# Optimization experiments

Hardware: AMD Instinct MI355X
Metric: run time of the kernel (lower is better)

The kernel has to match this reference:

```python
import jax, jax.numpy as jnp
import numpy as np

N_USERS = 200000
N_ITEMS = 100000
EMB_DIM = 64
N_LAYERS = 3
N_EDGES = 4000000
N_TOTAL = N_USERS + N_ITEMS


def setup_inputs() -> dict:
    key = jax.random.key(0)
    k1, k2, k3, k4 = jax.random.split(key, 4)
    # Xavier-uniform-ish init scale for embeddings
    lim = float(np.sqrt(6.0 / (N_USERS + EMB_DIM)))
    user_w = jax.random.uniform(k1, (N_USERS, EMB_DIM), jnp.float32, -lim, lim)
    lim_i = float(np.sqrt(6.0 / (N_ITEMS + EMB_DIM)))
    item_w = jax.random.uniform(k2, (N_ITEMS, EMB_DIM), jnp.float32, -lim_i, lim_i)
    src = jax.random.randint(k3, (N_EDGES,), 0, N_TOTAL, dtype=jnp.int32)
    dst = jax.random.randint(k4, (N_EDGES,), 0, N_TOTAL, dtype=jnp.int32)
    return {"user_w": user_w, "item_w": item_w, "src": src, "dst": dst}


def reference(user_w, item_w, src, dst):
    # x: [N_TOTAL, D] joint node embedding table
    x = jnp.concatenate([user_w, item_w], axis=0)
    # Row-degree of the COO adjacency (duplicates sum, same as coalesce)
    deg = jax.ops.segment_sum(jnp.ones_like(src, dtype=x.dtype), src,
                              num_segments=N_TOTAL)
    deg_inv_sqrt = jax.lax.rsqrt(deg + 1e-8)
    # Symmetric normalization weight per edge: d_i^-1/2 * d_j^-1/2
    w = (deg_inv_sqrt[src] * deg_inv_sqrt[dst])[:, None]  # [E, 1]

    h = x
    acc = x
    for _ in range(N_LAYERS):
        # SpMM: out[i] = sum_{(i,j) in E} w_ij * h[j]
        h = jax.ops.segment_sum(w * h[dst], src, num_segments=N_TOTAL)
        acc = acc + h
    out = acc / (N_LAYERS + 1)
    return out[:N_USERS], out[N_USERS:]
```

## Files before the change

kernel.cpp:

```cpp
#include <hip/hip_runtime.h>

#define N_USERS  200000
#define N_ITEMS  100000
#define N_TOTAL  300000
#define EMB_DIM  64
#define N_EDGES  4000000
#define N_LAYERS 3

#define SCAN_CHUNK 1024

#define B2_BITS 9
#define B2_ROWS (1 << B2_BITS)
#define NB2 ((N_TOTAL + B2_ROWS - 1) >> B2_BITS)
#define CHUNK_E 8192
#define NBLK ((N_EDGES + CHUNK_E - 1) / CHUNK_E)
#define NFLAT (NB2 * NBLK)
#define NSB_FLAT ((NFLAT + SCAN_CHUNK - 1) / SCAN_CHUNK)

#define DST_BITS 19
#define DST_MASK ((1 << DST_BITS) - 1)

typedef float f32x2 __attribute__((ext_vector_type(2)));

__device__ __forceinline__ unsigned bfpack(float a, float b) {
    unsigned ua = __float_as_uint(a); ua = (ua + 0x7fffu + ((ua >> 16) & 1u)) >> 16;
    unsigned ub = __float_as_uint(b); ub = (ub + 0x7fffu + ((ub >> 16) & 1u)) >> 16;
    return ua | (ub << 16);
}
__device__ __forceinline__ float bflo(unsigned u) { return __uint_as_float(u << 16); }
__device__ __forceinline__ float bfhi(unsigned u) { return __uint_as_float(u & 0xffff0000u); }
__device__ __forceinline__ f32x2 bf2(unsigned u) {
    f32x2 t; t.x = bflo(u); t.y = bfhi(u); return t;
}

__global__ void scanA_g(const int* __restrict__ in, int* __restrict__ out,
                        int* __restrict__ bsums, int n) {
    __shared__ int lds[256];
    int t = threadIdx.x, b = blockIdx.x;
    int base = b * SCAN_CHUNK + t * 4;
    int v[4];
#pragma unroll
    for (int k = 0; k < 4; ++k)
        v[k] = (base + k < n) ? in[base + k] : 0;
    int s = v[0] + v[1] + v[2] + v[3];
    lds[t] = s;
    __syncthreads();
    for (int off = 1; off < 256; off <<= 1) {
        int x = (t >= off) ? lds[t - off] : 0;
        __syncthreads();
        lds[t] += x;
        __syncthreads();
    }
    int inc = lds[t];
    int exc = inc - s;
    if (t == 255) bsums[b] = inc;
    int run = exc;
#pragma unroll
    for (int k = 0; k < 4; ++k) {
        if (base + k < n) out[base + k] = run;
        run += v[k];
    }
}

__global__ void scanB_g(int* __restrict__ bsums, int nb, int* __restrict__ total_out) {
    __shared__ int lds[512];
    int t = threadIdx.x;
    int v = (t < nb) ? bsums[t] : 0;
    lds[t] = v;
    __syncthreads();
    for (int o = 1; o < 512; o <<= 1) {
        int x = (t >= o) ? lds[t - o] : 0;
        __syncthreads();
        lds[t] += x;
        __syncthreads();
    }
    if (t < nb) bsums[t] = lds[t] - v;
    if (total_out && t == nb - 1) *total_out = lds[t];
}

__global__ __launch_bounds__(512) void partA_kernel(const int* __restrict__ src,
                                                    int* __restrict__ bcnt) {
    __shared__ int lcnt[NB2];
    int blk = blockIdx.x, t = threadIdx.x;
    for (int i = t; i < NB2; i += 512) lcnt[i] = 0;
    __syncthreads();
    int base = blk * CHUNK_E;
    int end = base + CHUNK_E; if (end > N_EDGES) end = N_EDGES;
    for (int e = base + 4 * t; e < end; e += 4 * 512) {
        int4 s4 = *(const int4*)(src + e);
        atomicAdd(&lcnt[s4.x >> B2_BITS], 1);
        atomicAdd(&lcnt[s4.y >> B2_BITS], 1);
        atomicAdd(&lcnt[s4.z >> B2_BITS], 1);
        atomicAdd(&lcnt[s4.w >> B2_BITS], 1);
    }
    __syncthreads();
    for (int i = t; i < NB2; i += 512)
        bcnt[(size_t)i * NBLK + blk] = lcnt[i];
}

__global__ __launch_bounds__(512) void partC_kernel(const int* __restrict__ src,
                                                    const int* __restrict__ dst,
                                                    const int* __restrict__ boffs,
                                                    const int* __restrict__ bs2,
                                                    int* __restrict__ edgebuf) {
    __shared__ int lcur[NB2];
    int blk = blockIdx.x, t = threadIdx.x;
    for (int i = t; i < NB2; i += 512) {
        size_t f = (size_t)i * NBLK + blk;
        lcur[i] = boffs[f] + bs2[f >> 10];
    }
    __syncthreads();
    int base = blk * CHUNK_E;
    int end = base + CHUNK_E; if (end > N_EDGES) end = N_EDGES;
    for (int e = base + 2 * t; e < end; e += 2 * 512) {
        int2 s2 = *(const int2*)(src + e);
        int2 d2 = *(const int2*)(dst + e);
        int pos0 = atomicAdd(&lcur[s2.x >> B2_BITS], 1);
        edgebuf[pos0] = ((s2.x & (B2_ROWS - 1)) << DST_BITS) | d2.x;
        int pos1 = atomicAdd(&lcur[s2.y >> B2_BITS], 1);
        edgebuf[pos1] = ((s2.y & (B2_ROWS - 1)) << DST_BITS) | d2.y;
    }
}

__global__ __launch_bounds__(512) void part2_kernel(const int* __restrict__ boffs,
                                                    const int* __restrict__ bs2,
                                                    const int* __restrict__ edgebuf,
                                                    int* __restrict__ col,
                                                    int* __restrict__ offs,
                                                    float* __restrict__ dinv) {
    __shared__ int lhist[B2_ROWS];
    __shared__ int lsums[512];
    int b = blockIdx.x;
    int base = b << B2_BITS;
    int nrows = N_TOTAL - base; if (nrows > B2_ROWS) nrows = B2_ROWS;
    int t = threadIdx.x;
    size_t f0 = (size_t)b * NBLK;
    int bstart = boffs[f0] + bs2[f0 >> 10];
    int eend;
    if (b + 1 < NB2) {
        size_t f1 = (size_t)(b + 1) * NBLK;
        eend = boffs[f1] + bs2[f1 >> 10];
    } else eend = N_EDGES;

    if (t < B2_ROWS) lhist[t] = 0;
    __syncthreads();
    for (int j = bstart + t; j < eend; j += 512)
        atomicAdd(&lhist[edgebuf[j] >> DST_BITS], 1);
    __syncthreads();
    int v = lhist[t];
    lsums[t] = v;
    __syncthreads();
    for (int o = 1; o < 512; o <<= 1) {
        int x = (t >= o) ? lsums[t - o] : 0;
        __syncthreads();
        lsums[t] += x;
        __syncthreads();
    }
    int o0 = bstart + lsums[t] - v;
    if (t < nrows) {
        offs[base + t] = o0;
        dinv[base + t] = rsqrtf((float)v + 1e-8f);
    }
    if (b == NB2 - 1 && t == 0) offs[N_TOTAL] = N_EDGES;
    lhist[t] = o0;
    __syncthreads();
    for (int j = bstart + t; j < eend; j += 512) {
        int e = edgebuf[j];
        int pos = atomicAdd(&lhist[e >> DST_BITS], 1);
        col[pos] = e & DST_MASK;
    }
}

__global__ void convert_kernel(const float4* __restrict__ uw4,
                               const float4* __restrict__ iw4,
                               const float* __restrict__ dinv,
                               uint2* __restrict__ g0) {
    int i = blockIdx.x * blockDim.x + threadIdx.x;
    const int n = (N_TOTAL + 1) * 16;
    if (i < n) {
        int row = i >> 4;
        if (row >= N_TOTAL) {
            g0[i] = make_uint2(0u, 0u);
        } else {
            float4 x = (row < N_USERS) ? uw4[i] : iw4[i - N_USERS * 16];
            float di = dinv[row];
            g0[i] = make_uint2(bfpack(di * x.x, di * x.y),
                               bfpack(di * x.z, di * x.w));
        }
    }
}

template <int MODE>
__global__ __launch_bounds__(256) void gather_kernel(
        const int* __restrict__ offs,
        const int* __restrict__ col,
        const float* __restrict__ dinv,
        const unsigned* __restrict__ gprev,
        unsigned* __restrict__ gnext,
        float4* __restrict__ out4,
        const float4* __restrict__ uw4,
        const float4* __restrict__ iw4) {
    int row  = blockIdx.x * 4 + (threadIdx.x >> 6);
    int lane = threadIdx.x & 63;
    int q    = lane >> 4;
    int r    = lane & 15;
    int start = __builtin_amdgcn_readfirstlane(offs[row]);
    int end   = __builtin_amdgcn_readfirstlane(offs[row + 1]);
    float di  = dinv[row];
    f32x2 acc01 = {0.f, 0.f};
    f32x2 acc23 = {0.f, 0.f};
    for (int cb = start; cb < end; cb += 64) {
        int rem = end - cb;
        int n = rem > 64 ? 64 : rem;
        int myc = (lane < rem) ? col[cb + lane] : N_TOTAL;
        for (int k0 = 0; k0 < n; k0 += 16) {
            int c0 = __shfl(myc, k0 + q);
            int c1 = __shfl(myc, k0 + 4 + q);
            int c2 = __shfl(myc, k0 + 8 + q);
            int c3 = __shfl(myc, k0 + 12 + q);
            uint2 u0 = *(const uint2*)(gprev + ((size_t)(unsigned)c0 << 5) + 2 * r);
            uint2 u1 = *(const uint2*)(gprev + ((size_t)(unsigned)c1 << 5) + 2 * r);
            uint2 u2 = *(const uint2*)(gprev + ((size_t)(unsigned)c2 << 5) + 2 * r);
            uint2 u3 = *(const uint2*)(gprev + ((size_t)(unsigned)c3 << 5) + 2 * r);
            acc01 += bf2(u0.x); acc23 += bf2(u0.y);
            acc01 += bf2(u1.x); acc23 += bf2(u1.y);
            acc01 += bf2(u2.x); acc23 += bf2(u2.y);
            acc01 += bf2(u3.x); acc23 += bf2(u3.y);
        }
    }
    float a0 = acc01.x, a1 = acc01.y, a2 = acc23.x, a3 = acc23.y;
    a0 += __shfl_xor(a0, 16);
    a1 += __shfl_xor(a1, 16);
    a2 += __shfl_xor(a2, 16);
    a3 += __shfl_xor(a3, 16);
    a0 += __shfl_xor(a0, 32);
    a1 += __shfl_xor(a1, 32);
    a2 += __shfl_xor(a2, 32);
    a3 += __shfl_xor(a3, 32);
    if (lane < 16) {
        float h0 = di * a0, h1 = di * a1, h2 = di * a2, h3 = di * a3;
        int p = row * 16 + r;
        if (MODE == 0) {
            float4 x = (row < N_USERS) ? uw4[p] : iw4[p - N_USERS * 16];
            ((uint2*)gnext)[p] = make_uint2(bfpack(di * h0, di * h1),
                                            bfpack(di * h2, di * h3));
            out4[p] = make_float4(x.x + h0, x.y + h1, x.z + h2, x.w + h3);
        } else if (MODE == 1) {
            float4 o = out4[p];
            ((uint2*)gnext)[p] = make_uint2(bfpack(di * h0, di * h1),
                                            bfpack(di * h2, di * h3));
            out4[p] = make_float4(o.x + h0, o.y + h1, o.z + h2, o.w + h3);
        } else {
            float4 o = out4[p];
            out4[p] = make_float4((o.x + h0) * 0.25f, (o.y + h1) * 0.25f,
                                  (o.z + h2) * 0.25f, (o.w + h3) * 0.25f);
        }
    }
    if (MODE != 2) {
        if (blockIdx.x == 0 && threadIdx.x < 32)
            gnext[N_TOTAL * 32 + threadIdx.x] = 0u;
    }
}

extern "C" void kernel_launch(void* const* d_in, const int* in_sizes, int n_in,
                              void* d_out, int out_size, void* d_ws, size_t ws_size,
                              hipStream_t stream) {
    const float* user_w = (const float*)d_in[0];
    const float* item_w = (const float*)d_in[1];
    const int*   src    = (const int*)d_in[2];
    const int*   dst    = (const int*)d_in[3];
    float* out = (float*)d_out;
    (void)in_sizes; (void)n_in; (void)out_size; (void)ws_size;

    char* ws = (char*)d_ws;
    size_t off = 0;
    auto alloc = [&](size_t bytes) {
        char* p = ws + off;
        off = (off + bytes + 255) & ~(size_t)255;
        return p;
    };
    int*      offs   = (int*)     alloc((size_t)(N_TOTAL + 1) * 4);
    int*      bcnt   = (int*)     alloc((size_t)NFLAT * 4);
    int*      boffs  = (int*)     alloc((size_t)NFLAT * 4);
    int*      bs2    = (int*)     alloc((size_t)NSB_FLAT * 4);
    int*      col    = (int*)     alloc((size_t)N_EDGES * 4);
    int*      edgebuf= (int*)     alloc((size_t)N_EDGES * 4);
    float*    dinv   = (float*)   alloc((size_t)N_TOTAL * 4);
    unsigned* g0     = (unsigned*)alloc((size_t)(N_TOTAL + 1) * 32 * 4);
    unsigned* g_a    = (unsigned*)alloc((size_t)(N_TOTAL + 1) * 32 * 4);
    unsigned* g_b    = (unsigned*)alloc((size_t)(N_TOTAL + 1) * 32 * 4);

    const int B = 256;
    const int gatherGrid = N_TOTAL / 4;

    partA_kernel<<<NBLK, 512, 0, stream>>>(src, bcnt);
    scanA_g<<<NSB_FLAT, B, 0, stream>>>(bcnt, boffs, bs2, NFLAT);
    scanB_g<<<1, 512, 0, stream>>>(bs2, NSB_FLAT, nullptr);
    partC_kernel<<<NBLK, 512, 0, stream>>>(src, dst, boffs, bs2, edgebuf);
    part2_kernel<<<NB2, 512, 0, stream>>>(boffs, bs2, edgebuf, col, offs, dinv);

    convert_kernel<<<((N_TOTAL + 1) * 16 + B - 1) / B, B, 0, stream>>>(
        (const float4*)user_w, (const float4*)item_w, dinv, (uint2*)g0);

    const float4* uw4 = (const float4*)user_w;
    const float4* iw4 = (const float4*)item_w;
    float4* out4 = (float4*)out;
    gather_kernel<0><<<gatherGrid, B, 0, stream>>>(offs, col, dinv, g0,  g_a, out4, uw4, iw4);
    gather_kernel<1><<<gatherGrid, B, 0, stream>>>(offs, col, dinv, g_a, g_b, out4, uw4, iw4);
    gather_kernel<2><<<gatherGrid, B, 0, stream>>>(offs, col, dinv, g_b, nullptr, out4, uw4, iw4);
}
```

Baseline: 573.9 us.

## Process four rows per wavefront with prefetched column indices; stage bucket edges in LDS

The gather kernel now assigns four consecutive rows to each wavefront, loading all row offsets and degree factors at once and prefetching the next row's column indices while the current row is processed. This is meant to hide the latency of the col load and offset reads that came before each row's feature gathers. Separately, part2 caches a bucket's edges in shared memory when they fit, so the second pass reads LDS instead of re-reading edgebuf from global memory. The costs are fewer waves in flight (grid reduced fourfold), more registers, and a 40KB LDS allocation in part2 that may lower its occupancy.

```diff
diff --git a/kernel.cpp b/kernel.cpp
--- a/kernel.cpp
+++ b/kernel.cpp
@@ -19,6 +19,10 @@
 
 #define DST_BITS 19
 #define DST_MASK ((1 << DST_BITS) - 1)
+
+#define P2_CAP 10240
+
+#define GR 4
 
 typedef float f32x2 __attribute__((ext_vector_type(2)));
 
@@ -130,6 +134,7 @@
                                                     float* __restrict__ dinv) {
     __shared__ int lhist[B2_ROWS];
     __shared__ int lsums[512];
+    __shared__ int lbuf[P2_CAP];
     int b = blockIdx.x;
     int base = b << B2_BITS;
     int nrows = N_TOTAL - base; if (nrows > B2_ROWS) nrows = B2_ROWS;
@@ -141,11 +146,21 @@
         size_t f1 = (size_t)(b + 1) * NBLK;
         eend = boffs[f1] + bs2[f1 >> 10];
     } else eend = N_EDGES;
+    int cnt = eend - bstart;
+    bool fits = (cnt <= P2_CAP);
 
     if (t < B2_ROWS) lhist[t] = 0;
     __syncthreads();
-    for (int j = bstart + t; j < eend; j += 512)
-        atomicAdd(&lhist[edgebuf[j] >> DST_BITS], 1);
+    if (fits) {
+        for (int j = t; j < cnt; j += 512) {
+            int e = edgebuf[bstart + j];
+            lbuf[j] = e;
+            atomicAdd(&lhist[e >> DST_BITS], 1);
+        }
+    } else {
+        for (int j = bstart + t; j < eend; j += 512)
+            atomicAdd(&lhist[edgebuf[j] >> DST_BITS], 1);
+    }
     __syncthreads();
     int v = lhist[t];
     lsums[t] = v;
@@ -164,10 +179,18 @@
     if (b == NB2 - 1 && t == 0) offs[N_TOTAL] = N_EDGES;
     lhist[t] = o0;
     __syncthreads();
-    for (int j = bstart + t; j < eend; j += 512) {
-        int e = edgebuf[j];
-        int pos = atomicAdd(&lhist[e >> DST_BITS], 1);
-        col[pos] = e & DST_MASK;
+    if (fits) {
+        for (int j = t; j < cnt; j += 512) {
+            int e = lbuf[j];
+            int pos = atomicAdd(&lhist[e >> DST_BITS], 1);
+            col[pos] = e & DST_MASK;
+        }
+    } else {
+        for (int j = bstart + t; j < eend; j += 512) {
+            int e = edgebuf[j];
+            int pos = atomicAdd(&lhist[e >> DST_BITS], 1);
+            col[pos] = e & DST_MASK;
+        }
     }
 }
 
@@ -200,24 +223,37 @@
         float4* __restrict__ out4,
         const float4* __restrict__ uw4,
         const float4* __restrict__ iw4) {
-    int row  = blockIdx.x * 4 + (threadIdx.x >> 6);
+    int wid  = blockIdx.x * 4 + (threadIdx.x >> 6);
+    int base_row = wid * GR;
     int lane = threadIdx.x & 63;
     int q    = lane >> 4;
     int r    = lane & 15;
-    int start = __builtin_amdgcn_readfirstlane(offs[row]);
-    int end   = __builtin_amdgcn_readfirstlane(offs[row + 1]);
-    float di  = dinv[row];
-    f32x2 acc01 = {0.f, 0.f};
-    f32x2 acc23 = {0.f, 0.f};
-    for (int cb = start; cb < end; cb += 64) {
-        int rem = end - cb;
-        int n = rem > 64 ? 64 : rem;
-        int myc = (lane < rem) ? col[cb + lane] : N_TOTAL;
+    int li = lane < GR ? lane : GR;
+    int off_l = offs[base_row + li];
+    float dv  = dinv[base_row + (lane < GR ? lane : GR - 1)];
+
+    int s0 = __builtin_amdgcn_readlane(off_l, 0);
+    int e0 = __builtin_amdgcn_readlane(off_l, 1);
+    int myc_cur = (lane < e0 - s0) ? col[s0 + lane] : N_TOTAL;
+
+#pragma unroll
+    for (int i = 0; i < GR; ++i) {
+        int start = __builtin_amdgcn_readlane(off_l, i);
+        int end   = __builtin_amdgcn_readlane(off_l, i + 1);
+        int myc_next = N_TOTAL;
+        if (i + 1 < GR) {
+            int sn = __builtin_amdgcn_readlane(off_l, i + 1);
+            int en = __builtin_amdgcn_readlane(off_l, i + 2);
+            myc_next = (lane < en - sn) ? col[sn + lane] : N_TOTAL;
+        }
+        f32x2 acc01 = {0.f, 0.f};
+        f32x2 acc23 = {0.f, 0.f};
+        int n = end - start; if (n > 64) n = 64;
         for (int k0 = 0; k0 < n; k0 += 16) {
-            int c0 = __shfl(myc, k0 + q);
-            int c1 = __shfl(myc, k0 + 4 + q);
-            int c2 = __shfl(myc, k0 + 8 + q);
-            int c3 = __shfl(myc, k0 + 12 + q);
+            int c0 = __shfl(myc_cur, k0 + q);
+            int c1 = __shfl(myc_cur, k0 + 4 + q);
+            int c2 = __shfl(myc_cur, k0 + 8 + q);
+            int c3 = __shfl(myc_cur, k0 + 12 + q);
             uint2 u0 = *(const uint2*)(gprev + ((size_t)(unsigned)c0 << 5) + 2 * r);
             uint2 u1 = *(const uint2*)(gprev + ((size_t)(unsigned)c1 << 5) + 2 * r);
             uint2 u2 = *(const uint2*)(gprev + ((size_t)(unsigned)c2 << 5) + 2 * r);
@@ -227,34 +263,56 @@
             acc01 += bf2(u2.x); acc23 += bf2(u2.y);
             acc01 += bf2(u3.x); acc23 += bf2(u3.y);
         }
-    }
-    float a0 = acc01.x, a1 = acc01.y, a2 = acc23.x, a3 = acc23.y;
-    a0 += __shfl_xor(a0, 16);
-    a1 += __shfl_xor(a1, 16);
-    a2 += __shfl_xor(a2, 16);
-    a3 += __shfl_xor(a3, 16);
-    a0 += __shfl_xor(a0, 32);
-    a1 += __shfl_xor(a1, 32);
-    a2 += __shfl_xor(a2, 32);
-    a3 += __shfl_xor(a3, 32);
-    if (lane < 16) {
-        float h0 = di * a0, h1 = di * a1, h2 = di * a2, h3 = di * a3;
-        int p = row * 16 + r;
-        if (MODE == 0) {
-            float4 x = (row < N_USERS) ? uw4[p] : iw4[p - N_USERS * 16];
-            ((uint2*)gnext)[p] = make_uint2(bfpack(di * h0, di * h1),
-                                            bfpack(di * h2, di * h3));
-            out4[p] = make_float4(x.x + h0, x.y + h1, x.z + h2, x.w + h3);
-        } else if (MODE == 1) {
-            float4 o = out4[p];
-            ((uint2*)gnext)[p] = make_uint2(bfpack(di * h0, di * h1),
-                                            bfpack(di * h2, di * h3));
-            out4[p] = make_float4(o.x + h0, o.y + h1, o.z + h2, o.w + h3);
-        } else {
-            float4 o = out4[p];
-            out4[p] = make_float4((o.x + h0) * 0.25f, (o.y + h1) * 0.25f,
-                                  (o.z + h2) * 0.25f, (o.w + h3) * 0.25f);
-        }
+        for (int cb = start + 64; cb < end; cb += 64) {
+            int rem = end - cb;
+            int nn = rem > 64 ? 64 : rem;
+            int myc = (lane < rem) ? col[cb + lane] : N_TOTAL;
+            for (int k0 = 0; k0 < nn; k0 += 16) {
+                int c0 = __shfl(myc, k0 + q);
+                int c1 = __shfl(myc, k0 + 4 + q);
+                int c2 = __shfl(myc, k0 + 8 + q);
+                int c3 = __shfl(myc, k0 + 12 + q);
+                uint2 u0 = *(const uint2*)(gprev + ((size_t)(unsigned)c0 << 5) + 2 * r);
+                uint2 u1 = *(const uint2*)(gprev + ((size_t)(unsigned)c1 << 5) + 2 * r);
+                uint2 u2 = *(const uint2*)(gprev + ((size_t)(unsigned)c2 << 5) + 2 * r);
+                uint2 u3 = *(const uint2*)(gprev + ((size_t)(unsigned)c3 << 5) + 2 * r);
+                acc01 += bf2(u0.x); acc23 += bf2(u0.y);
+                acc01 += bf2(u1.x); acc23 += bf2(u1.y);
+                acc01 += bf2(u2.x); acc23 += bf2(u2.y);
+                acc01 += bf2(u3.x); acc23 += bf2(u3.y);
+            }
+        }
+        float a0 = acc01.x, a1 = acc01.y, a2 = acc23.x, a3 = acc23.y;
+        a0 += __shfl_xor(a0, 16);
+        a1 += __shfl_xor(a1, 16);
+        a2 += __shfl_xor(a2, 16);
+        a3 += __shfl_xor(a3, 16);
+        a0 += __shfl_xor(a0, 32);
+        a1 += __shfl_xor(a1, 32);
+        a2 += __shfl_xor(a2, 32);
+        a3 += __shfl_xor(a3, 32);
+        float di = __shfl(dv, i);
+        if (lane < 16) {
+            int row = base_row + i;
+            float h0 = di * a0, h1 = di * a1, h2 = di * a2, h3 = di * a3;
+            int p = row * 16 + r;
+            if (MODE == 0) {
+                float4 x = (row < N_USERS) ? uw4[p] : iw4[p - N_USERS * 16];
+                ((uint2*)gnext)[p] = make_uint2(bfpack(di * h0, di * h1),
+                                                bfpack(di * h2, di * h3));
+                out4[p] = make_float4(x.x + h0, x.y + h1, x.z + h2, x.w + h3);
+            } else if (MODE == 1) {
+                float4 o = out4[p];
+                ((uint2*)gnext)[p] = make_uint2(bfpack(di * h0, di * h1),
+                                                bfpack(di * h2, di * h3));
+                out4[p] = make_float4(o.x + h0, o.y + h1, o.z + h2, o.w + h3);
+            } else {
+                float4 o = out4[p];
+                out4[p] = make_float4((o.x + h0) * 0.25f, (o.y + h1) * 0.25f,
+                                      (o.z + h2) * 0.25f, (o.w + h3) * 0.25f);
+            }
+        }
+        myc_cur = myc_next;
     }
     if (MODE != 2) {
         if (blockIdx.x == 0 && threadIdx.x < 32)
@@ -291,7 +349,7 @@
     unsigned* g_b    = (unsigned*)alloc((size_t)(N_TOTAL + 1) * 32 * 4);
 
     const int B = 256;
-    const int gatherGrid = N_TOTAL / 4;
+    const int gatherGrid = N_TOTAL / (4 * GR);
 
     partA_kernel<<<NBLK, 512, 0, stream>>>(src, bcnt);
     scanA_g<<<NSB_FLAT, B, 0, stream>>>(bcnt, boffs, bs2, NFLAT);
```

Result: faster. 535.7 us (-6.7%).
